# Performance work log

Hardware: AMD Instinct MI355X
Metric: run time of the kernel (lower is better)

## Reference

```python
import jax, jax.numpy as jnp
import numpy as np
from jax import lax

B, CIN, COUT, H, W = 4, 256, 256, 64, 64
K = 3  # kernel size
PAD = 1
STRIDE = 1


def setup_inputs() -> dict:
    key = jax.random.key(0)
    k1, k2, k3, k4 = jax.random.split(key, 4)
    x = jax.random.normal(k1, (B, CIN, H, W), dtype=jnp.float32)
    # small offset weights so learned offsets are modest (original init is zeros)
    offset_w = jax.random.normal(k2, (3 * K * K, CIN, K, K), dtype=jnp.float32) * 0.01
    offset_b = jax.random.normal(k3, (3 * K * K,), dtype=jnp.float32) * 0.01
    dcn_w = jax.random.normal(k4, (COUT, CIN, K, K), dtype=jnp.float32) * (1.0 / np.sqrt(CIN * K * K))
    return {"x": x, "offset_w": offset_w, "offset_b": offset_b, "dcn_w": dcn_w}


def _dcnv2(x, offset_w, offset_b, dcn_w):
    b, c, h, w = x.shape
    kk = K * K
    # offset conv (standard 3x3, stride 1, pad 1)
    o = lax.conv_general_dilated(
        x, offset_w, (STRIDE, STRIDE), ((PAD, PAD), (PAD, PAD)),
        dimension_numbers=("NCHW", "OIHW", "NCHW"))
    o = o + offset_b[None, :, None, None]
    ho, wo = o.shape[2], o.shape[3]
    off = o[:, : 2 * kk].reshape(b, kk, 2, ho, wo)  # pairs are (dy, dx)
    dy, dx = off[:, :, 0], off[:, :, 1]             # [b,kk,ho,wo]
    mask = jax.nn.sigmoid(o[:, 2 * kk:])            # [b,kk,ho,wo]

    ki, kj = jnp.meshgrid(jnp.arange(K), jnp.arange(K), indexing="ij")
    ki = ki.reshape(kk).astype(jnp.float32)
    kj = kj.reshape(kk).astype(jnp.float32)
    base_y = (jnp.arange(ho, dtype=jnp.float32) * STRIDE - PAD)[None, None, :, None] + ki[None, :, None, None]
    base_x = (jnp.arange(wo, dtype=jnp.float32) * STRIDE - PAD)[None, None, None, :] + kj[None, :, None, None]
    py = base_y + dy  # [b,kk,ho,wo] sampling y
    px = base_x + dx  # sampling x

    y0 = jnp.floor(py)
    x0 = jnp.floor(px)
    wy = py - y0  # bilinear fractional weights
    wx = px - x0
    y0i = y0.astype(jnp.int32)
    x0i = x0.astype(jnp.int32)

    xT = x.transpose(0, 2, 3, 1)  # [b,h,w,c] for channel-last gathers
    bidx = jnp.arange(b)[:, None, None, None]

    def gather(yi, xi):
        # zero padding outside the image
        valid = (yi >= 0) & (yi < h) & (xi >= 0) & (xi < w)
        yc = jnp.clip(yi, 0, h - 1)
        xc = jnp.clip(xi, 0, w - 1)
        v = xT[bidx, yc, xc]  # [b,kk,ho,wo,c]
        return v * valid[..., None].astype(x.dtype)

    g00 = gather(y0i, x0i)
    g01 = gather(y0i, x0i + 1)
    g10 = gather(y0i + 1, x0i)
    g11 = gather(y0i + 1, x0i + 1)

    wy_ = wy[..., None]
    wx_ = wx[..., None]
    sampled = (g00 * (1 - wy_) * (1 - wx_) + g01 * (1 - wy_) * wx_
               + g10 * wy_ * (1 - wx_) + g11 * wy_ * wx_)
    sampled = sampled * mask[..., None]  # modulation

    wk = dcn_w.reshape(dcn_w.shape[0], c, kk)  # [o,c,kk]
    return jnp.einsum("bkhwc,ock->bohw", sampled, wk)


def reference(x, offset_w, offset_b, dcn_w):
    return _dcnv2(x, offset_w, offset_b, dcn_w)
```

## Files before the change

kernel.cpp:

```cpp
#include <hip/hip_runtime.h>
#include <hip/hip_bf16.h>
#include <stdint.h>
#include <math.h>

#define KDIM 2304

typedef __attribute__((ext_vector_type(8))) short bf16x8;
typedef __attribute__((ext_vector_type(4))) float f32x4;

__device__ inline unsigned short f2bf(float f) {
  union { float f; unsigned int u; } v; v.f = f;
  unsigned int u = v.u;
  unsigned int r = (u + 0x7FFFu + ((u >> 16) & 1u)) >> 16;
  return (unsigned short)r;
}
__device__ inline float bf2f(unsigned short h) {
  union { unsigned int u; float f; } v; v.u = ((unsigned int)h) << 16;
  return v.f;
}

__device__ inline void gl2lds16(const void* g, void* l) {
  __builtin_amdgcn_global_load_lds((const __attribute__((address_space(1))) void*)g,
                                   (__attribute__((address_space(3))) void*)l,
                                   16, 0, 0);
}

__global__ __launch_bounds__(256) void k_prep(const float* __restrict__ x,
                                              unsigned short* __restrict__ xTb,
                                              const float* __restrict__ dcn_w,
                                              const float* __restrict__ offset_w,
                                              unsigned short* __restrict__ Wpk,
                                              unsigned short* __restrict__ Wob,
                                              unsigned short* __restrict__ zp) {
  __shared__ float tile[32][65];
  int bx = (int)blockIdx.x;
  int t = threadIdx.x;
  if (bx < 2048) {
    int pt = bx & 127, ct = (bx >> 7) & 3, b = bx >> 9;
    int p0 = pt * 32, c0 = ct * 64;
    const float* xb = x + ((size_t)b << 20);
#pragma unroll
    for (int i = 0; i < 2; ++i) {
      int idx = t + i * 256;
      int c = idx >> 3, pq = idx & 7;
      float4 v = *(const float4*)(xb + ((size_t)(c0 + c) << 12) + p0 + pq * 4);
      tile[pq * 4 + 0][c] = v.x;
      tile[pq * 4 + 1][c] = v.y;
      tile[pq * 4 + 2][c] = v.z;
      tile[pq * 4 + 3][c] = v.w;
    }
    __syncthreads();
    unsigned short* ob = xTb + ((size_t)b << 20);
#pragma unroll
    for (int i = 0; i < 2; ++i) {
      int idx = t + i * 256;
      int p = idx >> 4, cg = idx & 15;
      ushort4 o;
      o.x = f2bf(tile[p][cg * 4 + 0]);
      o.y = f2bf(tile[p][cg * 4 + 1]);
      o.z = f2bf(tile[p][cg * 4 + 2]);
      o.w = f2bf(tile[p][cg * 4 + 3]);
      *(ushort4*)(ob + (((size_t)(p0 + p)) << 8) + c0 + cg * 4) = o;
    }
  } else {
    int gid = (bx - 2048) * 256 + t;
    const int N1 = 72 * 8192;
    const int N2 = 32 * KDIM;
    if (gid < N1) {
      int j = gid & 7;
      int lane = (gid >> 3) & 63;
      int mb = (gid >> 9) & 15;
      int kc = gid >> 13;
      int row = mb * 16 + (lane & 15);
      int gk = kc * 32 + ((lane >> 4) << 3) + j;
      int c = gk & 255, kidx = gk >> 8;
      Wpk[gid] = f2bf(dcn_w[((size_t)(row * 256 + c)) * 9 + kidx]);
    } else if (gid < N1 + N2) {
      int g = gid - N1;
      int ch = g / KDIM, k = g % KDIM;
      int kidx = k >> 8, c = k & 255;
      Wob[g] = (ch < 27) ? f2bf(offset_w[((size_t)(ch * 256 + c)) * 9 + kidx])
                         : (unsigned short)0;
    } else if (gid < N1 + N2 + 128) {
      zp[gid - N1 - N2] = 0;
    }
  }
}

__global__ __launch_bounds__(256) void k_offs(const unsigned short* __restrict__ xTb,
                                              const unsigned short* __restrict__ Wob,
                                              const unsigned short* __restrict__ zp,
                                              const float* __restrict__ offb,
                                              float* __restrict__ SW) {
  __shared__ unsigned short As[4][32 * 32];
  __shared__ unsigned short Bs[4][32 * 32];
  __shared__ float Os[32][33];
  int t = threadIdx.x;
  int wv = t >> 6, lane = t & 63;
  int bid = (int)blockIdx.x;
  int swz = (bid & 7) * 64 + (bid >> 3);
  int n0 = swz * 32;

  int r0 = (t >> 2) & 31, coff = (t & 3) * 8;
  int rowA = n0 + r0;
  int b_ = rowA >> 12, hw = rowA & 4095, h = hw >> 6, w = hw & 63;
  int rB = ((t - 128) >> 2) & 31;

  f32x4 acc = {};

  auto stage = [&](int kt) {
    int buf = kt & 3;
    int k0 = kt * 32;
    int kidx = k0 >> 8, c0 = k0 & 255;
    if (t < 128) {
      int di = kidx / 3 - 1, dj = kidx % 3 - 1;
      int y = h + di, xx = w + dj;
      const unsigned short* g = (y >= 0 && y < 64 && xx >= 0 && xx < 64)
          ? xTb + (((((size_t)b_) << 12) + (y << 6) + xx) << 8) + c0 + coff
          : zp;
      gl2lds16(g, (char*)As[buf] + wv * 1024);
    } else {
      const unsigned short* gB = Wob + (size_t)rB * KDIM + k0 + coff;
      gl2lds16(gB, (char*)Bs[buf] + (wv - 2) * 1024);
    }
  };

  stage(0); stage(1); stage(2);

  int mf = wv & 1, nf = wv >> 1;
  for (int kt = 0; kt < 72; ++kt) {
    if (kt <= 69)      asm volatile("s_waitcnt vmcnt(2)" ::: "memory");
    else if (kt == 70) asm volatile("s_waitcnt vmcnt(1)" ::: "memory");
    else               asm volatile("s_waitcnt vmcnt(0)" ::: "memory");
    asm volatile("s_barrier" ::: "memory");
    if (kt + 3 < 72) stage(kt + 3);
    int buf = kt & 3;
    bf16x8 aF = *(const bf16x8*)(As[buf] + (mf * 16 + (lane & 15)) * 32 + (lane >> 4) * 8);
    bf16x8 bF = *(const bf16x8*)(Bs[buf] + (nf * 16 + (lane & 15)) * 32 + (lane >> 4) * 8);
    acc = __builtin_amdgcn_mfma_f32_16x16x32_bf16(aF, bF, acc, 0, 0, 0);
  }

  int quad = lane >> 4, cl = lane & 15;
#pragma unroll
  for (int r = 0; r < 4; ++r)
    Os[mf * 16 + quad * 4 + r][nf * 16 + cl] = acc[r];
  __syncthreads();

  for (int item = t; item < 288; item += 256) {
    int bl = item & 31, k = item >> 5;
    int bhw = n0 + bl;
    int h_ = (bhw >> 6) & 63, w_ = bhw & 63;
    float dy = Os[bl][2 * k]     + offb[2 * k];
    float dx = Os[bl][2 * k + 1] + offb[2 * k + 1];
    float mv = Os[bl][18 + k]    + offb[18 + k];
    float mask = 1.0f / (1.0f + expf(-mv));

    float py = (float)(h_ - 1 + k / 3) + dy;
    float px = (float)(w_ - 1 + k % 3) + dx;
    float y0f = floorf(py), x0f = floorf(px);
    float wy = py - y0f, wx = px - x0f;
    int y0 = (int)y0f, x0 = (int)x0f;
    int y1 = y0 + 1, x1 = x0 + 1;

    float vy0 = (y0 >= 0 && y0 < 64) ? 1.f : 0.f;
    float vy1 = (y1 >= 0 && y1 < 64) ? 1.f : 0.f;
    float vx0 = (x0 >= 0 && x0 < 64) ? 1.f : 0.f;
    float vx1 = (x1 >= 0 && x1 < 64) ? 1.f : 0.f;
    int y0c = min(max(y0, 0), 63), y1c = min(max(y1, 0), 63);
    int x0c = min(max(x0, 0), 63), x1c = min(max(x1, 0), 63);

    float4 wv4;
    wv4.x = (1.f - wy) * (1.f - wx) * vy0 * vx0 * mask;
    wv4.y = (1.f - wy) * wx * vy0 * vx1 * mask;
    wv4.z = wy * (1.f - wx) * vy1 * vx0 * mask;
    wv4.w = wy * wx * vy1 * vx1 * mask;
    uint4 ov;
    ov.x = (unsigned)(((y0c << 6) + x0c) << 8);
    ov.y = (unsigned)(((y0c << 6) + x1c) << 8);
    ov.z = (unsigned)(((y1c << 6) + x0c) << 8);
    ov.w = (unsigned)(((y1c << 6) + x1c) << 8);

    float* p = SW + (size_t)(k * 16384 + bhw) * 8;
    *(float4*)p = wv4;
    *(uint4*)(p + 4) = ov;
  }
}

#define FSTEP(KT, Q, AF, BUF, DOSW)                                            \
  do {                                                                         \
    float s0_ = wv4.x * bf2f(Q[0].x) + wv4.y * bf2f(Q[1].x) +                  \
                wv4.z * bf2f(Q[2].x) + wv4.w * bf2f(Q[3].x);                   \
    float s1_ = wv4.x * bf2f(Q[0].y) + wv4.y * bf2f(Q[1].y) +                  \
                wv4.z * bf2f(Q[2].y) + wv4.w * bf2f(Q[3].y);                   \
    float s2_ = wv4.x * bf2f(Q[0].z) + wv4.y * bf2f(Q[1].z) +                  \
                wv4.z * bf2f(Q[2].z) + wv4.w * bf2f(Q[3].z);                   \
    float s3_ = wv4.x * bf2f(Q[0].w) + wv4.y * bf2f(Q[1].w) +                  \
                wv4.z * bf2f(Q[2].w) + wv4.w * bf2f(Q[3].w);                   \
    union { __hip_bfloat162 h2[2]; ushort4 v; } pk_;                           \
    pk_.h2[0] = __float22bfloat162_rn(make_float2(s0_, s1_));                  \
    pk_.h2[1] = __float22bfloat162_rn(make_float2(s2_, s3_));                  \
    *(ushort4*)(&Bs[BUF][bsw]) = pk_.v;                                        \
    if (DOSW && ((KT) & 7) == 0 && (KT) < 64) {                                \
      const float* swp_ =                                                      \
          SW + ((size_t)(((((KT) >> 3) + 1) << 14) + n0 + r)) * 8;             \
      wv4n = *(const float4*)swp_;                                             \
      ovn  = *(const uint4*)(swp_ + 4);                                        \
    }                                                                          \
    if ((KT) < 70) {                                                           \
      int kn_ = (KT) + 2;                                                      \
      uint4 o_ = (((KT) & 7) >= 6) ? ovn : ov;                                 \
      unsigned c_ = (unsigned)(((kn_ & 7) << 5) + ch0);                        \
      Q[0] = *(const ushort4*)(xb + o_.x + c_);                                \
      Q[1] = *(const ushort4*)(xb + o_.y + c_);                                \
      Q[2] = *(const ushort4*)(xb + o_.z + c_);                                \
      Q[3] = *(const ushort4*)(xb + o_.w + c_);                                \
    }                                                                          \
    asm volatile("s_waitcnt lgkmcnt(0)\n\ts_barrier" ::: "memory");            \
    bf16x8 bF0_ = *(const bf16x8*)(&Bs[BUF][(wn * 32 + (lane & 15)) * 40 +     \
                                            (lane >> 4) * 8]);                 \
    bf16x8 bF1_ = *(const bf16x8*)(&Bs[BUF][(wn * 32 + 16 + (lane & 15)) * 40 +\
                                            (lane >> 4) * 8]);                 \
    _Pragma("unroll")                                                          \
    for (int i_ = 0; i_ < 4; ++i_) {                                           \
      acc[i_][0] =                                                             \
          __builtin_amdgcn_mfma_f32_16x16x32_bf16(AF[i_], bF0_, acc[i_][0],    \
                                                  0, 0, 0);                    \
      acc[i_][1] =                                                             \
          __builtin_amdgcn_mfma_f32_16x16x32_bf16(AF[i_], bF1_, acc[i_][1],    \
                                                  0, 0, 0);                    \
    }                                                                          \
    if ((KT) < 70) {                                                           \
      int kn_ = (KT) + 2;                                                      \
      _Pragma("unroll")                                                        \
      for (int i_ = 0; i_ < 4; ++i_)                                           \
        AF[i_] = *(const bf16x8*)(wpBase + ((size_t)kn_ * 16 + i_) * 512);     \
    }                                                                          \
  } while (0)

__global__ __launch_bounds__(512) void k_fused(const unsigned short* __restrict__ Wpk,
                                               const unsigned short* __restrict__ xTb,
                                               const float* __restrict__ SW,
                                               float* __restrict__ out) {
  __shared__ __align__(16) unsigned short Bs[2][64 * 40];
  int t = threadIdx.x;
  int wv = t >> 6, lane = t & 63;
  int wm = wv & 3, wn = wv >> 2;
  int bid = (int)blockIdx.x;
  int swz = (bid & 7) * 32 + (bid >> 3);
  int n0 = swz * 64;
  int b  = n0 >> 12;
  const unsigned short* xb = xTb + ((size_t)b << 20);

  int r = t >> 3, g = t & 7;
  int ch0 = g * 4;
  int bsw = r * 40 + ch0;

  const unsigned short* wpBase = Wpk + ((size_t)(wm * 4 * 64 + lane)) * 8;

  f32x4 acc[4][2] = {};

  float4 wv4, wv4n; uint4 ov, ovn;
  {
    const float* sw = SW + ((size_t)(n0 + r)) * 8;
    wv4 = *(const float4*)sw;
    ov  = *(const uint4*)(sw + 4);
  }
  wv4n = wv4; ovn = ov;

  ushort4 qA[4], qB[4];
  bf16x8 aFA[4], aFB[4];

  {
    unsigned c0_ = (unsigned)ch0;
    qA[0] = *(const ushort4*)(xb + ov.x + c0_);
    qA[1] = *(const ushort4*)(xb + ov.y + c0_);
    qA[2] = *(const ushort4*)(xb + ov.z + c0_);
    qA[3] = *(const ushort4*)(xb + ov.w + c0_);
    unsigned c1_ = (unsigned)(32 + ch0);
    qB[0] = *(const ushort4*)(xb + ov.x + c1_);
    qB[1] = *(const ushort4*)(xb + ov.y + c1_);
    qB[2] = *(const ushort4*)(xb + ov.z + c1_);
    qB[3] = *(const ushort4*)(xb + ov.w + c1_);
#pragma unroll
    for (int i = 0; i < 4; ++i) {
      aFA[i] = *(const bf16x8*)(wpBase + (size_t)i * 512);
      aFB[i] = *(const bf16x8*)(wpBase + (size_t)(16 + i) * 512);
    }
  }

  for (int kt = 0; kt < 72; kt += 2) {
    FSTEP(kt,     qA, aFA, 0, 1);
    FSTEP(kt + 1, qB, aFB, 1, 0);
    if ((kt & 7) == 6) { wv4 = wv4n; ov = ovn; }
  }

  int quad = lane >> 4, cl = lane & 15;
  float* ob = out + (((size_t)b) << 20);
#pragma unroll
  for (int i = 0; i < 4; ++i) {
    int mbase = wm * 64 + i * 16 + quad * 4;
#pragma unroll
    for (int j = 0; j < 2; ++j) {
      int hw = (n0 & 4095) + wn * 32 + j * 16 + cl;
      float* op = ob + hw;
#pragma unroll
      for (int rr = 0; rr < 4; ++rr)
        op[((size_t)(mbase + rr)) << 12] = acc[i][j][rr];
    }
  }
}

extern "C" void kernel_launch(void* const* d_in, const int* in_sizes, int n_in,
                              void* d_out, int out_size, void* d_ws, size_t ws_size,
                              hipStream_t stream) {
  const float* x        = (const float*)d_in[0];
  const float* offset_w = (const float*)d_in[1];
  const float* offset_b = (const float*)d_in[2];
  const float* dcn_w    = (const float*)d_in[3];
  float* out = (float*)d_out;

  char* ws = (char*)d_ws;
  size_t off = 0;
  auto carve = [&](size_t bytes) -> void* {
    void* p = ws + off;
    off += (bytes + 255) & ~(size_t)255;
    return p;
  };
  unsigned short* xTb = (unsigned short*)carve(4ull * 64 * 64 * 256 * 2);
  unsigned short* Wpk = (unsigned short*)carve(72ull * 8192 * 2);
  unsigned short* Wob = (unsigned short*)carve(32ull * KDIM * 2);
  unsigned short* zp  = (unsigned short*)carve(256);
  float*          SW  = (float*)carve(9ull * 16384 * 8 * 4);
  (void)ws_size; (void)in_sizes; (void)n_in; (void)out_size;

  const int WPREP_BLOCKS = (72 * 8192 + 32 * KDIM + 128 + 255) / 256;
  k_prep<<<dim3(2048 + WPREP_BLOCKS), 256, 0, stream>>>(
      x, xTb, dcn_w, offset_w, Wpk, Wob, zp);
  k_offs<<<dim3(512), 256, 0, stream>>>(xTb, Wob, zp, offset_b, SW);
  k_fused<<<dim3(256), 512, 0, stream>>>(Wpk, xTb, SW, out);
}
```

Baseline: 142.9 us.

## Process two K-tiles per barrier phase with 16-byte gathers and doubled LDS stage

Restructures the fused deformable-conv GEMM loop so each pipeline phase covers two 32-wide K slices instead of one. Each thread now gathers 8 bf16 channels per corner with 16-byte loads and writes a bf16x8 to LDS. This halves the number of barriers and issues 16 MFMAs per barrier instead of 8. It also doubles the register-held weight fragments (8 per buffer) and the LDS staging, and adds launch_bounds(512,2), which may force register spilling under the higher register demand.

```diff
diff --git a/kernel.cpp b/kernel.cpp
--- a/kernel.cpp
+++ b/kernel.cpp
@@ -186,62 +186,64 @@
   }
 }
 
-#define FSTEP(KT, Q, AF, BUF, DOSW)                                            \
+#define PHASE(PH, Q, AF, BUF)                                                  \
   do {                                                                         \
-    float s0_ = wv4.x * bf2f(Q[0].x) + wv4.y * bf2f(Q[1].x) +                  \
-                wv4.z * bf2f(Q[2].x) + wv4.w * bf2f(Q[3].x);                   \
-    float s1_ = wv4.x * bf2f(Q[0].y) + wv4.y * bf2f(Q[1].y) +                  \
-                wv4.z * bf2f(Q[2].y) + wv4.w * bf2f(Q[3].y);                   \
-    float s2_ = wv4.x * bf2f(Q[0].z) + wv4.y * bf2f(Q[1].z) +                  \
-                wv4.z * bf2f(Q[2].z) + wv4.w * bf2f(Q[3].z);                   \
-    float s3_ = wv4.x * bf2f(Q[0].w) + wv4.y * bf2f(Q[1].w) +                  \
-                wv4.z * bf2f(Q[2].w) + wv4.w * bf2f(Q[3].w);                   \
-    union { __hip_bfloat162 h2[2]; ushort4 v; } pk_;                           \
-    pk_.h2[0] = __float22bfloat162_rn(make_float2(s0_, s1_));                  \
-    pk_.h2[1] = __float22bfloat162_rn(make_float2(s2_, s3_));                  \
-    *(ushort4*)(&Bs[BUF][bsw]) = pk_.v;                                        \
-    if (DOSW && ((KT) & 7) == 0 && (KT) < 64) {                                \
+    float s_[8];                                                               \
+    _Pragma("unroll")                                                          \
+    for (int j_ = 0; j_ < 8; ++j_)                                             \
+      s_[j_] = wv4.x * bf2f((unsigned short)Q[0][j_]) +                        \
+               wv4.y * bf2f((unsigned short)Q[1][j_]) +                        \
+               wv4.z * bf2f((unsigned short)Q[2][j_]) +                        \
+               wv4.w * bf2f((unsigned short)Q[3][j_]);                         \
+    union { __hip_bfloat162 h2[4]; bf16x8 v; } pk_;                            \
+    pk_.h2[0] = __float22bfloat162_rn(make_float2(s_[0], s_[1]));              \
+    pk_.h2[1] = __float22bfloat162_rn(make_float2(s_[2], s_[3]));              \
+    pk_.h2[2] = __float22bfloat162_rn(make_float2(s_[4], s_[5]));              \
+    pk_.h2[3] = __float22bfloat162_rn(make_float2(s_[6], s_[7]));              \
+    *(bf16x8*)(&Bs[BUF][s_th][bsw]) = pk_.v;                                   \
+    if (((PH) & 3) == 0 && (PH) < 32) {                                        \
       const float* swp_ =                                                      \
-          SW + ((size_t)(((((KT) >> 3) + 1) << 14) + n0 + r)) * 8;             \
+          SW + ((size_t)((((PH) >> 2) + 1) * 16384 + n0 + r)) * 8;             \
       wv4n = *(const float4*)swp_;                                             \
       ovn  = *(const uint4*)(swp_ + 4);                                        \
     }                                                                          \
-    if ((KT) < 70) {                                                           \
-      int kn_ = (KT) + 2;                                                      \
-      uint4 o_ = (((KT) & 7) >= 6) ? ovn : ov;                                 \
-      unsigned c_ = (unsigned)(((kn_ & 7) << 5) + ch0);                        \
-      Q[0] = *(const ushort4*)(xb + o_.x + c_);                                \
-      Q[1] = *(const ushort4*)(xb + o_.y + c_);                                \
-      Q[2] = *(const ushort4*)(xb + o_.z + c_);                                \
-      Q[3] = *(const ushort4*)(xb + o_.w + c_);                                \
+    if ((PH) < 34) {                                                           \
+      int kn0_ = 2 * (PH) + 4;                                                 \
+      uint4 o_ = (((PH) & 3) >= 2) ? ovn : ov;                                 \
+      unsigned c_ = (unsigned)((((kn0_ & 7) + s_th) << 5) + gg * 8);           \
+      Q[0] = *(const bf16x8*)(xb + o_.x + c_);                                 \
+      Q[1] = *(const bf16x8*)(xb + o_.y + c_);                                 \
+      Q[2] = *(const bf16x8*)(xb + o_.z + c_);                                 \
+      Q[3] = *(const bf16x8*)(xb + o_.w + c_);                                 \
     }                                                                          \
     asm volatile("s_waitcnt lgkmcnt(0)\n\ts_barrier" ::: "memory");            \
-    bf16x8 bF0_ = *(const bf16x8*)(&Bs[BUF][(wn * 32 + (lane & 15)) * 40 +     \
-                                            (lane >> 4) * 8]);                 \
-    bf16x8 bF1_ = *(const bf16x8*)(&Bs[BUF][(wn * 32 + 16 + (lane & 15)) * 40 +\
-                                            (lane >> 4) * 8]);                 \
     _Pragma("unroll")                                                          \
-    for (int i_ = 0; i_ < 4; ++i_) {                                           \
-      acc[i_][0] =                                                             \
-          __builtin_amdgcn_mfma_f32_16x16x32_bf16(AF[i_], bF0_, acc[i_][0],    \
-                                                  0, 0, 0);                    \
-      acc[i_][1] =                                                             \
-          __builtin_amdgcn_mfma_f32_16x16x32_bf16(AF[i_], bF1_, acc[i_][1],    \
-                                                  0, 0, 0);                    \
+    for (int s2_ = 0; s2_ < 2; ++s2_) {                                        \
+      bf16x8 bF0_ = *(const bf16x8*)(                                          \
+          &Bs[BUF][s2_][(wn * 32 + (lane & 15)) * 56 + (lane >> 4) * 8]);      \
+      bf16x8 bF1_ = *(const bf16x8*)(                                          \
+          &Bs[BUF][s2_][(wn * 32 + 16 + (lane & 15)) * 56 + (lane >> 4) * 8]); \
+      _Pragma("unroll")                                                        \
+      for (int i_ = 0; i_ < 4; ++i_) {                                         \
+        acc[i_][0] = __builtin_amdgcn_mfma_f32_16x16x32_bf16(                  \
+            AF[s2_ * 4 + i_], bF0_, acc[i_][0], 0, 0, 0);                      \
+        acc[i_][1] = __builtin_amdgcn_mfma_f32_16x16x32_bf16(                  \
+            AF[s2_ * 4 + i_], bF1_, acc[i_][1], 0, 0, 0);                      \
+      }                                                                        \
     }                                                                          \
-    if ((KT) < 70) {                                                           \
-      int kn_ = (KT) + 2;                                                      \
+    if ((PH) < 34) {                                                           \
       _Pragma("unroll")                                                        \
-      for (int i_ = 0; i_ < 4; ++i_)                                           \
-        AF[i_] = *(const bf16x8*)(wpBase + ((size_t)kn_ * 16 + i_) * 512);     \
+      for (int i_ = 0; i_ < 8; ++i_)                                           \
+        AF[i_] = *(const bf16x8*)(                                             \
+            wpBase + ((size_t)((2 * (PH) + 4 + (i_ >> 2)) * 16 + (i_ & 3))) * 512); \
     }                                                                          \
   } while (0)
 
-__global__ __launch_bounds__(512) void k_fused(const unsigned short* __restrict__ Wpk,
-                                               const unsigned short* __restrict__ xTb,
-                                               const float* __restrict__ SW,
-                                               float* __restrict__ out) {
-  __shared__ __align__(16) unsigned short Bs[2][64 * 40];
+__global__ __launch_bounds__(512, 2) void k_fused(const unsigned short* __restrict__ Wpk,
+                                                  const unsigned short* __restrict__ xTb,
+                                                  const float* __restrict__ SW,
+                                                  float* __restrict__ out) {
+  __shared__ __align__(16) unsigned short Bs[2][2][64 * 56];
   int t = threadIdx.x;
   int wv = t >> 6, lane = t & 63;
   int wm = wv & 3, wn = wv >> 2;
@@ -251,9 +253,10 @@
   int b  = n0 >> 12;
   const unsigned short* xb = xTb + ((size_t)b << 20);
 
-  int r = t >> 3, g = t & 7;
-  int ch0 = g * 4;
-  int bsw = r * 40 + ch0;
+  int r = t >> 3;
+  int u = t & 7;
+  int s_th = u & 1, gg = u >> 1;
+  int bsw = r * 56 + gg * 8;
 
   const unsigned short* wpBase = Wpk + ((size_t)(wm * 4 * 64 + lane)) * 8;
 
@@ -267,31 +270,31 @@
   }
   wv4n = wv4; ovn = ov;
 
-  ushort4 qA[4], qB[4];
-  bf16x8 aFA[4], aFB[4];
+  bf16x8 qA[4], qB[4];
+  bf16x8 aFA[8], aFB[8];
 
   {
-    unsigned c0_ = (unsigned)ch0;
-    qA[0] = *(const ushort4*)(xb + ov.x + c0_);
-    qA[1] = *(const ushort4*)(xb + ov.y + c0_);
-    qA[2] = *(const ushort4*)(xb + ov.z + c0_);
-    qA[3] = *(const ushort4*)(xb + ov.w + c0_);
-    unsigned c1_ = (unsigned)(32 + ch0);
-    qB[0] = *(const ushort4*)(xb + ov.x + c1_);
-    qB[1] = *(const ushort4*)(xb + ov.y + c1_);
-    qB[2] = *(const ushort4*)(xb + ov.z + c1_);
-    qB[3] = *(const ushort4*)(xb + ov.w + c1_);
-#pragma unroll
-    for (int i = 0; i < 4; ++i) {
-      aFA[i] = *(const bf16x8*)(wpBase + (size_t)i * 512);
-      aFB[i] = *(const bf16x8*)(wpBase + (size_t)(16 + i) * 512);
-    }
-  }
-
-  for (int kt = 0; kt < 72; kt += 2) {
-    FSTEP(kt,     qA, aFA, 0, 1);
-    FSTEP(kt + 1, qB, aFB, 1, 0);
-    if ((kt & 7) == 6) { wv4 = wv4n; ov = ovn; }
+    unsigned cA = (unsigned)((s_th << 5) + gg * 8);
+    unsigned cB = (unsigned)(((2 + s_th) << 5) + gg * 8);
+    qA[0] = *(const bf16x8*)(xb + ov.x + cA);
+    qA[1] = *(const bf16x8*)(xb + ov.y + cA);
+    qA[2] = *(const bf16x8*)(xb + ov.z + cA);
+    qA[3] = *(const bf16x8*)(xb + ov.w + cA);
+    qB[0] = *(const bf16x8*)(xb + ov.x + cB);
+    qB[1] = *(const bf16x8*)(xb + ov.y + cB);
+    qB[2] = *(const bf16x8*)(xb + ov.z + cB);
+    qB[3] = *(const bf16x8*)(xb + ov.w + cB);
+#pragma unroll
+    for (int i = 0; i < 8; ++i) {
+      aFA[i] = *(const bf16x8*)(wpBase + ((size_t)(((i >> 2)) * 16 + (i & 3))) * 512);
+      aFB[i] = *(const bf16x8*)(wpBase + ((size_t)((2 + (i >> 2)) * 16 + (i & 3))) * 512);
+    }
+  }
+
+  for (int ph = 0; ph < 36; ph += 2) {
+    PHASE(ph,     qA, aFA, 0);
+    PHASE(ph + 1, qB, aFB, 1);
+    if ((ph & 3) == 2) { wv4 = wv4n; ov = ovn; }
   }
 
   int quad = lane >> 4, cl = lane & 15;
```

Result: faster. 135.6 us (-5.1%).
